# Optimization experiments

Measured on AMD Instinct MI355X. Metric: run time of the kernel, lower is better.

The kernel has to match this reference:

```python
import jax, jax.numpy as jnp
import numpy as np

B, H, W = 32768, 28, 28
HID = 800


def dft2(x):
    # centered 2D DFT: fftshift(fft2(ifftshift(x)))
    ax = (-2, -1)
    return jnp.fft.fftshift(jnp.fft.fft2(jnp.fft.ifftshift(x, axes=ax), axes=ax), axes=ax)


def idft2(x):
    ax = (-2, -1)
    return jnp.fft.fftshift(jnp.fft.ifft2(jnp.fft.ifftshift(x, axes=ax), axes=ax), axes=ax)


def setup_inputs() -> dict:
    key = jax.random.key(0)
    k = jax.random.split(key, 5)
    x = jax.random.normal(k[0], (B, H, W), dtype=jnp.float32)
    tmask_re = jnp.ones((1, H, W), dtype=jnp.float32)
    tmask_im = jnp.zeros((1, H, W), dtype=jnp.float32)
    w1 = jax.random.normal(k[1], (HID, H * W), dtype=jnp.float32) * 0.03
    b1 = jax.random.normal(k[2], (HID,), dtype=jnp.float32) * 0.03
    w4 = jax.random.normal(k[3], (10, HID), dtype=jnp.float32) * 0.03
    b4 = jax.random.normal(k[4], (10,), dtype=jnp.float32) * 0.03
    return {"x": x, "tmask_re": tmask_re, "tmask_im": tmask_im,
            "w1": w1, "b1": b1, "w4": w4, "b4": b4}


def reference(x, tmask_re, tmask_im, w1, b1, w4, b4):
    tmask = jax.lax.complex(tmask_re, tmask_im)          # [1,28,28] complex64
    xf = dft2(x.astype(jnp.complex64))                    # [B,28,28] complex64
    xf = tmask * xf                                       # elementwise complex mask
    xr = jnp.real(idft2(xf))                              # back to real image
    h = xr.reshape(-1, H * W)                             # [B,784]
    h = jax.nn.relu(h @ w1.T + b1)                        # [B,800]
    logits = h @ w4.T + b4                                # [B,10]
    return jax.nn.log_softmax(logits, axis=-1)
```

## Files before the change

kernel.cpp:

```cpp
#include <hip/hip_runtime.h>
#include <hip/hip_bf16.h>
#include <cmath>

typedef unsigned short u16;
typedef __attribute__((ext_vector_type(8))) short short8v;
typedef __attribute__((ext_vector_type(8))) unsigned short ushort8v;
typedef __attribute__((ext_vector_type(4))) float f32x4;

#define NPIX 784
#define KP   800
#define NH   800
#define LSTR 424

__device__ __forceinline__ u16 f2bf(float f) {
    union { float f; unsigned int u; } v; v.f = f;
    unsigned int u = v.u;
    unsigned int r = (u + 0x7FFFu + ((u >> 16) & 1u)) >> 16;
    return (u16)r;
}

__device__ __forceinline__ short8v cvt8(f32x4 v0, f32x4 v1) {
    union { __hip_bfloat162 h; ushort2 u; } a, b, c, d;
    a.h = __float22bfloat162_rn(make_float2(v0[0], v0[1]));
    b.h = __float22bfloat162_rn(make_float2(v0[2], v0[3]));
    c.h = __float22bfloat162_rn(make_float2(v1[0], v1[1]));
    d.h = __float22bfloat162_rn(make_float2(v1[2], v1[3]));
    short8v r;
    r[0] = (short)a.u.x; r[1] = (short)a.u.y; r[2] = (short)b.u.x; r[3] = (short)b.u.y;
    r[4] = (short)c.u.x; r[5] = (short)c.u.y; r[6] = (short)d.u.x; r[7] = (short)d.u.y;
    return r;
}

__global__ void k_kre(const float* __restrict__ MRE, const float* __restrict__ MIM,
                      float* __restrict__ KRE, float* __restrict__ FLAG)
{
    __shared__ float msre[784], msim[784], tre[784], tim[784];
    __shared__ float c28[28], s28[28];
    __shared__ int smax;

    const int t = threadIdx.x;
    if (t < 28) {
        float th = (float)t * (6.283185307179586f / 28.0f);
        s28[t] = sinf(th);
        c28[t] = cosf(th);
    }
    if (t == 0) smax = 0;
    if (t < 784) {
        int r = t / 28, c = t - r * 28;
        int idx = ((r + 14) % 28) * 28 + ((c + 14) % 28);
        msre[t] = MRE[idx];
        msim[t] = MIM[idx];
    }
    __syncthreads();
    if (t < 784) {
        int u = t / 28, cc = t - u * 28;
        float re = 0.f, im = 0.f;
        int ph = 0;
        for (int v = 0; v < 28; ++v) {
            float cr = c28[ph], ci = s28[ph];
            float ar = msre[u * 28 + v], ai = msim[u * 28 + v];
            re += ar * cr - ai * ci;
            im += ar * ci + ai * cr;
            ph += cc; if (ph >= 28) ph -= 28;
        }
        tre[t] = re; tim[t] = im;
    }
    __syncthreads();
    float dev = 0.f;
    if (t < 784) {
        int pr = t / 28, pc = t - pr * 28;
        float s = 0.f;
        int ph = 0;
        for (int u = 0; u < 28; ++u) {
            s += tre[u * 28 + pc] * c28[ph] - tim[u * 28 + pc] * s28[ph];
            ph += pr; if (ph >= 28) ph -= 28;
        }
        s *= (1.0f / 784.0f);
        KRE[t] = s;
        dev = fabsf(s - (t == 0 ? 1.0f : 0.0f));
    }
    #pragma unroll
    for (int m = 32; m >= 1; m >>= 1) dev = fmaxf(dev, __shfl_xor(dev, m, 64));
    if ((t & 63) == 0) atomicMax(&smax, __float_as_int(dev));
    __syncthreads();
    if (t == 0) FLAG[0] = (__int_as_float(smax) < 1e-4f) ? 1.0f : 0.0f;
}

__global__ void k_w1pack(const float* __restrict__ W1, const float* __restrict__ KRE,
                         const float* __restrict__ FLAG, u16* __restrict__ W1P)
{
    const int c = blockIdx.x;
    const int t = threadIdx.x;
    const bool delta = (FLAG[0] > 0.5f);
    __shared__ float w1d[56 * 56];
    __shared__ float kr[784];

    if (delta) {
        if (t < 100) {
            int k0 = t * 8;
            ushort8v h;
            if (k0 + 7 < NPIX) {
                const float4* wp = (const float4*)(W1 + (size_t)c * NPIX + k0);
                float4 a = wp[0], b = wp[1];
                h[0] = f2bf(a.x); h[1] = f2bf(a.y); h[2] = f2bf(a.z); h[3] = f2bf(a.w);
                h[4] = f2bf(b.x); h[5] = f2bf(b.y); h[6] = f2bf(b.z); h[7] = f2bf(b.w);
            } else {
                #pragma unroll
                for (int e = 0; e < 8; ++e) {
                    int k = k0 + e;
                    h[e] = (k < NPIX) ? f2bf(W1[(size_t)c * NPIX + k]) : (u16)0;
                }
            }
            int kf = k0 >> 5, r = k0 & 31;
            int l  = ((r >> 3) << 4) | (c & 15);
            int nf = c >> 4;
            ((ushort8v*)W1P)[(nf * 25 + kf) * 64 + l] = h;
        }
        return;
    }
    for (int i = t; i < 784; i += 128) kr[i] = KRE[i];
    for (int i = t; i < 3136; i += 128) {
        int r = i / 56, cc = i - r * 56;
        w1d[i] = W1[(size_t)c * NPIX + (r % 28) * 28 + (cc % 28)];
    }
    __syncthreads();
    for (int k = t; k < KP; k += 128) {
        float v = 0.f;
        if (k < NPIX) {
            int krr = k / 28, kcc = k - krr * 28;
            for (int dr = 0; dr < 28; ++dr) {
                const float* wrow = &w1d[(krr + dr) * 56 + kcc];
                const float* krow = &kr[dr * 28];
                #pragma unroll 4
                for (int dc = 0; dc < 28; ++dc) v += wrow[dc] * krow[dc];
            }
        }
        int kf = k >> 5, r = k & 31;
        int l  = ((r >> 3) << 4) | (c & 15);
        int nf = c >> 4;
        W1P[(size_t)(((nf * 25 + kf) * 64 + l) << 3) | (r & 7)] = f2bf(v);
    }
}

__global__ void k_w4pack2(const float* __restrict__ W4, u16* __restrict__ W4P2)
{
    int i = blockIdx.x * 256 + threadIdx.x;
    if (i >= 1920) return;
    int l = i & 63, wk = i >> 6;
    int w = wk / 3, kt2 = wk - w * 3;
    int lc = l & 15, lk = l >> 4;
    ushort8v h;
    #pragma unroll
    for (int e = 0; e < 8; ++e) {
        int k = w * 80 + kt2 * 32 + lk * 8 + e;
        h[e] = (lc < 10 && k < 800) ? f2bf(W4[lc * NH + k]) : (u16)0;
    }
    ((ushort8v*)W4P2)[i] = h;
}

__global__ __launch_bounds__(640) __attribute__((amdgpu_waves_per_eu(3, 3)))
void k_main(
    const float* __restrict__ X, const u16* __restrict__ W1P,
    const u16* __restrict__ W4P2, const float* __restrict__ B1,
    const float* __restrict__ B4, float* __restrict__ OUT)
{
    __shared__ __align__(16) u16 As[64 * LSTR];
    const int t = threadIdx.x;
    const int row0 = blockIdx.x * 64;
    const int l = t & 63, w = t >> 6;
    const int lc = l & 15, lk = l >> 4;

    f32x4 acc[4][5];
    #pragma unroll
    for (int m = 0; m < 4; ++m)
        #pragma unroll
        for (int n = 0; n < 5; ++n) acc[m][n] = (f32x4)(0.0f);

    const short8v* BP = (const short8v*)W1P;
    short8v bb[2][5];
    #pragma unroll
    for (int n = 0; n < 5; ++n)
        bb[0][n] = BP[((w * 5 + n) * 25 + 0) * 64 + l];

    #pragma unroll
    for (int i = 0; i < 5; ++i) {
        int u = t + 640 * i;
        if (i < 4 || u < 3072) {
            int row = u / 48, uc = u - row * 48;
            const float* g = X + (size_t)(row0 + row) * NPIX + uc * 8;
            f32x4 v0 = *(const f32x4*)(g);
            f32x4 v1 = *(const f32x4*)(g + 4);
            *(short8v*)(As + row * LSTR + uc * 8) = cvt8(v0, v1);
        }
    }
    asm volatile("s_waitcnt lgkmcnt(0)" ::: "memory");
    __builtin_amdgcn_s_barrier();
    __builtin_amdgcn_sched_barrier(0);

    #pragma unroll
    for (int kt = 0; kt < 12; ++kt) {
        #pragma unroll
        for (int n = 0; n < 5; ++n)
            bb[(kt + 1) & 1][n] = BP[((w * 5 + n) * 25 + (kt + 1)) * 64 + l];
        const u16* ab = As + lc * LSTR + kt * 32 + lk * 8;
        __builtin_amdgcn_s_setprio(1);
        #pragma unroll
        for (int m = 0; m < 4; ++m) {
            short8v a = *(const short8v*)(ab + m * (16 * LSTR));
            #pragma unroll
            for (int n = 0; n < 5; ++n)
                acc[m][n] = __builtin_amdgcn_mfma_f32_16x16x32_bf16(a, bb[kt & 1][n], acc[m][n], 0, 0, 0);
        }
        __builtin_amdgcn_s_setprio(0);
    }
    asm volatile("s_waitcnt lgkmcnt(0)" ::: "memory");
    __builtin_amdgcn_s_barrier();
    __builtin_amdgcn_sched_barrier(0);

    #pragma unroll
    for (int i = 0; i < 6; ++i) {
        int u = t + 640 * i;
        if (i < 5 || u < 3328) {
            int row = u / 52, uc = u - row * 52;
            int gcol = 384 + uc * 8;
            short8v hv;
            if (gcol < NPIX) {
                const float* g = X + (size_t)(row0 + row) * NPIX + gcol;
                f32x4 v0 = *(const f32x4*)(g);
                f32x4 v1 = *(const f32x4*)(g + 4);
                hv = cvt8(v0, v1);
            } else {
                hv = (short8v)(0);
            }
            *(short8v*)(As + row * LSTR + uc * 8) = hv;
        }
    }
    asm volatile("s_waitcnt lgkmcnt(0)" ::: "memory");
    __builtin_amdgcn_s_barrier();
    __builtin_amdgcn_sched_barrier(0);

    #pragma unroll
    for (int kt = 12; kt < 25; ++kt) {
        if (kt < 24) {
            #pragma unroll
            for (int n = 0; n < 5; ++n)
                bb[(kt + 1) & 1][n] = BP[((w * 5 + n) * 25 + (kt + 1)) * 64 + l];
        }
        const u16* ab = As + lc * LSTR + (kt - 12) * 32 + lk * 8;
        __builtin_amdgcn_s_setprio(1);
        #pragma unroll
        for (int m = 0; m < 4; ++m) {
            short8v a = *(const short8v*)(ab + m * (16 * LSTR));
            #pragma unroll
            for (int n = 0; n < 5; ++n)
                acc[m][n] = __builtin_amdgcn_mfma_f32_16x16x32_bf16(a, bb[kt & 1][n], acc[m][n], 0, 0, 0);
        }
        __builtin_amdgcn_s_setprio(0);
    }
    asm volatile("s_waitcnt lgkmcnt(0)" ::: "memory");
    __builtin_amdgcn_s_barrier();
    __builtin_amdgcn_sched_barrier(0);

    u16* strip = As + w * 1536;
    {
        uint2 z = make_uint2(0u, 0u);
        *(uint2*)((char*)strip + (l >> 2) * 192 + 160 + (l & 3) * 8) = z;
    }
    float bn[5];
    #pragma unroll
    for (int n = 0; n < 5; ++n) bn[n] = B1[w * 80 + n * 16 + lc];
    const short8v* WP = (const short8v*)W4P2;
    short8v w4f[3];
    #pragma unroll
    for (int kt2 = 0; kt2 < 3; ++kt2)
        w4f[kt2] = WP[(w * 3 + kt2) * 64 + l];

    f32x4 pc[4];
    #pragma unroll
    for (int m = 0; m < 4; ++m) {
        #pragma unroll
        for (int n = 0; n < 5; ++n)
            #pragma unroll
            for (int j = 0; j < 4; ++j)
                strip[(lk * 4 + j) * 96 + n * 16 + lc] = f2bf(fmaxf(acc[m][n][j] + bn[n], 0.0f));
        pc[m] = (f32x4)(0.0f);
        #pragma unroll
        for (int kt2 = 0; kt2 < 3; ++kt2) {
            short8v a2 = *(const short8v*)(strip + lc * 96 + kt2 * 32 + lk * 8);
            pc[m] = __builtin_amdgcn_mfma_f32_16x16x32_bf16(a2, w4f[kt2], pc[m], 0, 0, 0);
        }
    }
    __syncthreads();

    float* PLf = (float*)As + w * 640;
    if (lc < 10) {
        #pragma unroll
        for (int m = 0; m < 4; ++m)
            #pragma unroll
            for (int j = 0; j < 4; ++j)
                PLf[(m * 16 + lk * 4 + j) * 10 + lc] = pc[m][j];
    }
    __syncthreads();

    if (t < 64) {
        float lg[10];
        #pragma unroll
        for (int o = 0; o < 10; ++o) lg[o] = B4[o];
        #pragma unroll
        for (int w2 = 0; w2 < 10; ++w2) {
            const float* PLw = (const float*)As + w2 * 640;
            #pragma unroll
            for (int o = 0; o < 10; ++o) lg[o] += PLw[t * 10 + o];
        }
        float mx = lg[0];
        #pragma unroll
        for (int o = 1; o < 10; ++o) mx = fmaxf(mx, lg[o]);
        float se = 0.f;
        #pragma unroll
        for (int o = 0; o < 10; ++o) se += expf(lg[o] - mx);
        float lse = logf(se);
        float* op = OUT + (size_t)(row0 + t) * 10;
        #pragma unroll
        for (int o = 0; o < 10; ++o) op[o] = lg[o] - mx - lse;
    }
}

extern "C" void kernel_launch(void* const* d_in, const int* in_sizes, int n_in,
                              void* d_out, int out_size, void* d_ws, size_t ws_size,
                              hipStream_t stream)
{
    const float* X   = (const float*)d_in[0];
    const float* MRE = (const float*)d_in[1];
    const float* MIM = (const float*)d_in[2];
    const float* W1  = (const float*)d_in[3];
    const float* B1  = (const float*)d_in[4];
    const float* W4  = (const float*)d_in[5];
    const float* B4  = (const float*)d_in[6];
    float* OUT = (float*)d_out;

    float* kre  = (float*)d_ws;
    float* flag = kre + 784;
    u16*   w1p  = (u16*)((char*)d_ws + 4096);
    u16*   w4p2 = (u16*)((char*)d_ws + 4096 + 1310720);

    k_kre<<<1, 832, 0, stream>>>(MRE, MIM, kre, flag);
    k_w1pack<<<800, 128, 0, stream>>>(W1, kre, flag, w1p);
    k_w4pack2<<<8, 256, 0, stream>>>(W4, w4p2);
    k_main<<<512, 640, 0, stream>>>(X, w1p, w4p2, B1, B4, OUT);
}
```

Measured before the change: 68.83 us.

## Process two row tiles per block with async LDS prefetch of second tile

Each block now handles 128 rows as two 64-row tiles, halving the grid to 256 blocks. While the first tile's GEMM runs, the first half of the second tile's fp32 input is prefetched straight into a large swizzled LDS buffer with global_load_lds. It is then converted to bf16 on the fly from LDS during the second tile's MMA loop. This hides input load latency, but it raises LDS use to about 149 KB per block and leaves fewer blocks than CUs on a 256-CU part.

```diff
diff --git a/kernel.cpp b/kernel.cpp
--- a/kernel.cpp
+++ b/kernel.cpp
@@ -11,6 +11,7 @@
 #define KP   800
 #define NH   800
 #define LSTR 424
+#define B32OFF 54272
 
 __device__ __forceinline__ u16 f2bf(float f) {
     union { float f; unsigned int u; } v; v.f = f;
@@ -29,6 +30,13 @@
     r[0] = (short)a.u.x; r[1] = (short)a.u.y; r[2] = (short)b.u.x; r[3] = (short)b.u.y;
     r[4] = (short)c.u.x; r[5] = (short)c.u.y; r[6] = (short)d.u.x; r[7] = (short)d.u.y;
     return r;
+}
+
+__device__ __forceinline__ void gload16(const float* g, char* l) {
+    __builtin_amdgcn_global_load_lds(
+        (const __attribute__((address_space(1))) unsigned int*)g,
+        (__attribute__((address_space(3))) unsigned int*)l,
+        16, 0, 0);
 }
 
 __global__ void k_kre(const float* __restrict__ MRE, const float* __restrict__ MIM,
@@ -158,15 +166,87 @@
     ((ushort8v*)W4P2)[i] = h;
 }
 
+__device__ __forceinline__ void tail_epilogue(
+    f32x4 (&acc)[4][5], u16* As, const float* __restrict__ B1,
+    const short8v* __restrict__ WP, const float* __restrict__ B4,
+    float* __restrict__ OUT, int rowbase, int t, int w, int l, int lc, int lk)
+{
+    u16* strip = As + w * 1536;
+    {
+        uint2 z = make_uint2(0u, 0u);
+        *(uint2*)((char*)strip + (l >> 2) * 192 + 160 + (l & 3) * 8) = z;
+    }
+    float bn[5];
+    #pragma unroll
+    for (int n = 0; n < 5; ++n) bn[n] = B1[w * 80 + n * 16 + lc];
+    short8v w4f[3];
+    #pragma unroll
+    for (int kt2 = 0; kt2 < 3; ++kt2)
+        w4f[kt2] = WP[(w * 3 + kt2) * 64 + l];
+
+    f32x4 pc[4];
+    #pragma unroll
+    for (int m = 0; m < 4; ++m) {
+        #pragma unroll
+        for (int n = 0; n < 5; ++n)
+            #pragma unroll
+            for (int j = 0; j < 4; ++j)
+                strip[(lk * 4 + j) * 96 + n * 16 + lc] = f2bf(fmaxf(acc[m][n][j] + bn[n], 0.0f));
+        pc[m] = (f32x4)(0.0f);
+        #pragma unroll
+        for (int kt2 = 0; kt2 < 3; ++kt2) {
+            short8v a2 = *(const short8v*)(strip + lc * 96 + kt2 * 32 + lk * 8);
+            pc[m] = __builtin_amdgcn_mfma_f32_16x16x32_bf16(a2, w4f[kt2], pc[m], 0, 0, 0);
+        }
+    }
+    __syncthreads();
+
+    float* PLf = (float*)As + w * 640;
+    if (lc < 10) {
+        #pragma unroll
+        for (int m = 0; m < 4; ++m)
+            #pragma unroll
+            for (int j = 0; j < 4; ++j)
+                PLf[(m * 16 + lk * 4 + j) * 10 + lc] = pc[m][j];
+    }
+    __syncthreads();
+
+    if (t < 64) {
+        float lg[10];
+        #pragma unroll
+        for (int o = 0; o < 10; ++o) lg[o] = B4[o];
+        #pragma unroll
+        for (int w2 = 0; w2 < 10; ++w2) {
+            const float* PLw = (const float*)As + w2 * 640;
+            #pragma unroll
+            for (int o = 0; o < 10; ++o) lg[o] += PLw[t * 10 + o];
+        }
+        float mx = lg[0];
+        #pragma unroll
+        for (int o = 1; o < 10; ++o) mx = fmaxf(mx, lg[o]);
+        float se = 0.f;
+        #pragma unroll
+        for (int o = 0; o < 10; ++o) se += expf(lg[o] - mx);
+        float lse = logf(se);
+        float* op = OUT + (size_t)(rowbase + t) * 10;
+        #pragma unroll
+        for (int o = 0; o < 10; ++o) op[o] = lg[o] - mx - lse;
+    }
+    __syncthreads();
+}
+
 __global__ __launch_bounds__(640) __attribute__((amdgpu_waves_per_eu(3, 3)))
 void k_main(
     const float* __restrict__ X, const u16* __restrict__ W1P,
     const u16* __restrict__ W4P2, const float* __restrict__ B1,
     const float* __restrict__ B4, float* __restrict__ OUT)
 {
-    __shared__ __align__(16) u16 As[64 * LSTR];
+    __shared__ __align__(16) char SMEM[152576];
+    u16*  As   = (u16*)SMEM;
+    char* b32  = SMEM + B32OFF;
+
     const int t = threadIdx.x;
-    const int row0 = blockIdx.x * 64;
+    const int row0 = blockIdx.x * 128;
     const int l = t & 63, w = t >> 6;
     const int lc = l & 15, lk = l >> 4;
 
@@ -177,10 +257,15 @@
         for (int n = 0; n < 5; ++n) acc[m][n] = (f32x4)(0.0f);
 
     const short8v* BP = (const short8v*)W1P;
+    const short8v* WP = (const short8v*)W4P2;
     short8v bb[2][5];
     #pragma unroll
     for (int n = 0; n < 5; ++n)
         bb[0][n] = BP[((w * 5 + n) * 25 + 0) * 64 + l];
+
+    int pr_row = t / 96;
+    int pr_rem = t - pr_row * 96;
+    const char* x2b = (const char*)(X + (size_t)(row0 + 64) * NPIX);
 
     #pragma unroll
     for (int i = 0; i < 5; ++i) {
@@ -202,6 +287,15 @@
         #pragma unroll
         for (int n = 0; n < 5; ++n)
             bb[(kt + 1) & 1][n] = BP[((w * 5 + n) * 25 + (kt + 1)) * 64 + l];
+        if (kt < 10) {
+            if (kt < 9 || t < 384) {
+                int bcol = (pr_rem * 16) ^ ((pr_row & 7) << 4);
+                gload16((const float*)(x2b + (size_t)pr_row * 3136 + bcol),
+                        b32 + 16 * t + kt * 10240);
+            }
+            pr_row += 6; pr_rem += 64;
+            if (pr_rem >= 96) { pr_rem -= 96; pr_row += 1; }
+        }
         const u16* ab = As + lc * LSTR + kt * 32 + lk * 8;
         __builtin_amdgcn_s_setprio(1);
         #pragma unroll
@@ -257,72 +351,92 @@
         }
         __builtin_amdgcn_s_setprio(0);
     }
-    asm volatile("s_waitcnt lgkmcnt(0)" ::: "memory");
-    __builtin_amdgcn_s_barrier();
-    __builtin_amdgcn_sched_barrier(0);
-
-    u16* strip = As + w * 1536;
-    {
-        uint2 z = make_uint2(0u, 0u);
-        *(uint2*)((char*)strip + (l >> 2) * 192 + 160 + (l & 3) * 8) = z;
-    }
-    float bn[5];
-    #pragma unroll
-    for (int n = 0; n < 5; ++n) bn[n] = B1[w * 80 + n * 16 + lc];
-    const short8v* WP = (const short8v*)W4P2;
-    short8v w4f[3];
-    #pragma unroll
-    for (int kt2 = 0; kt2 < 3; ++kt2)
-        w4f[kt2] = WP[(w * 3 + kt2) * 64 + l];
-
-    f32x4 pc[4];
-    #pragma unroll
-    for (int m = 0; m < 4; ++m) {
+    #pragma unroll
+    for (int n = 0; n < 5; ++n)
+        bb[0][n] = BP[((w * 5 + n) * 25 + 0) * 64 + l];
+
+    asm volatile("s_waitcnt lgkmcnt(0)" ::: "memory");
+    __builtin_amdgcn_s_barrier();
+    __builtin_amdgcn_sched_barrier(0);
+
+    tail_epilogue(acc, As, B1, WP, B4, OUT, row0, t, w, l, lc, lk);
+
+    #pragma unroll
+    for (int m = 0; m < 4; ++m)
+        #pragma unroll
+        for (int n = 0; n < 5; ++n) acc[m][n] = (f32x4)(0.0f);
+
+    asm volatile("s_waitcnt vmcnt(0)" ::: "memory");
+    __builtin_amdgcn_s_barrier();
+    __builtin_amdgcn_sched_barrier(0);
+
+    const int aq0 = (lk * 32) ^ ((lc & 7) << 4);
+    #pragma unroll
+    for (int kt = 0; kt < 12; ++kt) {
         #pragma unroll
         for (int n = 0; n < 5; ++n)
-            #pragma unroll
-            for (int j = 0; j < 4; ++j)
-                strip[(lk * 4 + j) * 96 + n * 16 + lc] = f2bf(fmaxf(acc[m][n][j] + bn[n], 0.0f));
-        pc[m] = (f32x4)(0.0f);
-        #pragma unroll
-        for (int kt2 = 0; kt2 < 3; ++kt2) {
-            short8v a2 = *(const short8v*)(strip + lc * 96 + kt2 * 32 + lk * 8);
-            pc[m] = __builtin_amdgcn_mfma_f32_16x16x32_bf16(a2, w4f[kt2], pc[m], 0, 0, 0);
-        }
-    }
-    __syncthreads();
-
-    float* PLf = (float*)As + w * 640;
-    if (lc < 10) {
-        #pragma unroll
-        for (int m = 0; m < 4; ++m)
-            #pragma unroll
-            for (int j = 0; j < 4; ++j)
-                PLf[(m * 16 + lk * 4 + j) * 10 + lc] = pc[m][j];
-    }
-    __syncthreads();
-
-    if (t < 64) {
-        float lg[10];
-        #pragma unroll
-        for (int o = 0; o < 10; ++o) lg[o] = B4[o];
-        #pragma unroll
-        for (int w2 = 0; w2 < 10; ++w2) {
-            const float* PLw = (const float*)As + w2 * 640;
-            #pragma unroll
-            for (int o = 0; o < 10; ++o) lg[o] += PLw[t * 10 + o];
-        }
-        float mx = lg[0];
-        #pragma unroll
-        for (int o = 1; o < 10; ++o) mx = fmaxf(mx, lg[o]);
-        float se = 0.f;
-        #pragma unroll
-        for (int o = 0; o < 10; ++o) se += expf(lg[o] - mx);
-        float lse = logf(se);
-        float* op = OUT + (size_t)(row0 + t) * 10;
-        #pragma unroll
-        for (int o = 0; o < 10; ++o) op[o] = lg[o] - mx - lse;
-    }
+            bb[(kt + 1) & 1][n] = BP[((w * 5 + n) * 25 + (kt + 1)) * 64 + l];
+        const char* ab = b32 + lc * 1536 + kt * 128;
+        __builtin_amdgcn_s_setprio(1);
+        #pragma unroll
+        for (int m = 0; m < 4; ++m) {
+            f32x4 v0 = *(const f32x4*)(ab + m * 24576 + aq0);
+            f32x4 v1 = *(const f32x4*)(ab + m * 24576 + (aq0 ^ 16));
+            short8v a = cvt8(v0, v1);
+            #pragma unroll
+            for (int n = 0; n < 5; ++n)
+                acc[m][n] = __builtin_amdgcn_mfma_f32_16x16x32_bf16(a, bb[kt & 1][n], acc[m][n], 0, 0, 0);
+        }
+        __builtin_amdgcn_s_setprio(0);
+    }
+    __builtin_amdgcn_s_barrier();
+    __builtin_amdgcn_sched_barrier(0);
+
+    #pragma unroll
+    for (int i = 0; i < 6; ++i) {
+        int u = t + 640 * i;
+        if (i < 5 || u < 3328) {
+            int row = u / 52, uc = u - row * 52;
+            int gcol = 384 + uc * 8;
+            short8v hv;
+            if (gcol < NPIX) {
+                const float* g = X + (size_t)(row0 + 64 + row) * NPIX + gcol;
+                f32x4 v0 = *(const f32x4*)(g);
+                f32x4 v1 = *(const f32x4*)(g + 4);
+                hv = cvt8(v0, v1);
+            } else {
+                hv = (short8v)(0);
+            }
+            *(short8v*)(As + row * LSTR + uc * 8) = hv;
+        }
+    }
+    asm volatile("s_waitcnt lgkmcnt(0)" ::: "memory");
+    __builtin_amdgcn_s_barrier();
+    __builtin_amdgcn_sched_barrier(0);
+
+    #pragma unroll
+    for (int kt = 12; kt < 25; ++kt) {
+        if (kt < 24) {
+            #pragma unroll
+            for (int n = 0; n < 5; ++n)
+                bb[(kt + 1) & 1][n] = BP[((w * 5 + n) * 25 + (kt + 1)) * 64 + l];
+        }
+        const u16* ab = As + lc * LSTR + (kt - 12) * 32 + lk * 8;
+        __builtin_amdgcn_s_setprio(1);
+        #pragma unroll
+        for (int m = 0; m < 4; ++m) {
+            short8v a = *(const short8v*)(ab + m * (16 * LSTR));
+            #pragma unroll
+            for (int n = 0; n < 5; ++n)
+                acc[m][n] = __builtin_amdgcn_mfma_f32_16x16x32_bf16(a, bb[kt & 1][n], acc[m][n], 0, 0, 0);
+        }
+        __builtin_amdgcn_s_setprio(0);
+    }
+    asm volatile("s_waitcnt lgkmcnt(0)" ::: "memory");
+    __builtin_amdgcn_s_barrier();
+    __builtin_amdgcn_sched_barrier(0);
+
+    tail_epilogue(acc, As, B1, WP, B4, OUT, row0 + 64, t, w, l, lc, lk);
 }
 
 extern "C" void kernel_launch(void* const* d_in, const int* in_sizes, int n_in,
@@ -346,5 +460,5 @@
     k_kre<<<1, 832, 0, stream>>>(MRE, MIM, kre, flag);
     k_w1pack<<<800, 128, 0, stream>>>(W1, kre, flag, w1p);
     k_w4pack2<<<8, 256, 0, stream>>>(W4, w4p2);
-    k_main<<<512, 640, 0, stream>>>(X, w1p, w4p2, B1, B4, OUT);
-}
+    k_main<<<256, 640, 0, stream>>>(X, w1p, w4p2, B1, B4, OUT);
+}
```

Result: slower. 223.6 us (+224.9%).
